# Kernel tuning notes

Measured on AMD Instinct MI355X. Metric: run time of the kernel, lower is better.

The kernel has to match this reference:

```python
import jax, jax.numpy as jnp
import numpy as np

HIDDEN = 1024


def setup_inputs() -> dict:
    key = jax.random.key(0)
    ks = jax.random.split(key, 8)
    x_in, y_in, out_dim, hidden = 1024, 1024, 1024, HIDDEN
    Nx, Ny = 4096, 4096
    s = lambda d: 1.0 / np.sqrt(d)
    return {
        "x": jax.random.normal(ks[0], (Nx, x_in), jnp.float32),
        "y": jax.random.normal(ks[1], (Ny, y_in), jnp.float32),
        "Wq": jax.random.normal(ks[2], (hidden, x_in), jnp.float32) * s(x_in),
        "bq": jnp.zeros((hidden,), jnp.float32),
        "Wk": jax.random.normal(ks[3], (hidden, y_in), jnp.float32) * s(y_in),
        "bk": jnp.zeros((hidden,), jnp.float32),
        "Wv": jax.random.normal(ks[4], (out_dim, y_in), jnp.float32) * s(y_in),
        "bv": jnp.zeros((out_dim,), jnp.float32),
    }


def reference(x, y, Wq, bq, Wk, bk, Wv, bv):
    # Linear projections (torch Linear: x @ W.T + b)
    q = x @ Wq.T + bq          # [Nx, H]
    k = y @ Wk.T + bk          # [Ny, H]
    v = y @ Wv.T + bv          # [Ny, D_out]
    scores = (q @ k.T) / jnp.sqrt(jnp.asarray(HIDDEN, q.dtype))  # [Nx, Ny]
    attn = jax.nn.softmax(scores, axis=1)
    return attn @ v            # [Nx, D_out]
```

## Files before the change

### kernel.cpp

```cpp
#include <hip/hip_runtime.h>
#include <cstdint>
#include <cstddef>

typedef __attribute__((ext_vector_type(8))) __bf16 bf16x8;
typedef __attribute__((ext_vector_type(4))) float  f32x4;

#define WAITCNT_VM(n) ((n & 0xF) | 0x70 | 0xF00 | (((n) >> 4) << 14))

__device__ __forceinline__ unsigned short f32_to_bf16(float f) {
    union { float f; unsigned int u; } cv;
    cv.f = f;
    unsigned int u = cv.u;
    return (unsigned short)((u + 0x7fffu + ((u >> 16) & 1u)) >> 16);
}

__device__ __forceinline__ float bf16_to_f32(unsigned short h) {
    union { unsigned int u; float f; } cv;
    cv.u = ((unsigned int)h) << 16;
    return cv.f;
}

__device__ __forceinline__ void async_copy16(const unsigned short* g, unsigned short* lds) {
    __builtin_amdgcn_global_load_lds(
        (const __attribute__((address_space(1))) unsigned int*)g,
        (__attribute__((address_space(3))) unsigned int*)lds,
        16, 0, 0);
}

__global__ __launch_bounds__(256) void cast_all(
    const float* __restrict__ x,  const float* __restrict__ y,
    const float* __restrict__ wq, const float* __restrict__ wk, const float* __restrict__ wv,
    unsigned short* __restrict__ xb,  unsigned short* __restrict__ yb,
    unsigned short* __restrict__ wqb, unsigned short* __restrict__ wkb,
    unsigned short* __restrict__ wvb, float* __restrict__ lsum)
{
    int b = blockIdx.x;
    if (b >= 11264) {
        float4 z = {0.f, 0.f, 0.f, 0.f};
#pragma unroll
        for (int t = 0; t < 4; ++t)
            ((float4*)lsum)[threadIdx.x * 4 + t] = z;
        return;
    }
    const float* s; unsigned short* d; int base;
    if      (b < 4096)  { s = x;  d = xb;  base = b; }
    else if (b < 8192)  { s = y;  d = yb;  base = b - 4096; }
    else if (b < 9216)  { s = wq; d = wqb; base = b - 8192; }
    else if (b < 10240) { s = wk; d = wkb; base = b - 9216; }
    else                { s = wv; d = wvb; base = b - 10240; }
    int i = base * 256 + threadIdx.x;
    float4 v = ((const float4*)s)[i];
    ushort4 o;
    o.x = f32_to_bf16(v.x);
    o.y = f32_to_bf16(v.y);
    o.z = f32_to_bf16(v.z);
    o.w = f32_to_bf16(v.w);
    ((ushort4*)d)[i] = o;
}

__device__ __forceinline__ void gemm_core_pf(
    const unsigned short* __restrict__ A, const unsigned short* __restrict__ B,
    int K, int rowBase, int colBase, int kBeg, int kEnd,
    unsigned short* ldsA, unsigned short* ldsB, f32x4 acc[4][4])
{
    const int tid  = threadIdx.x;
    const int lane = tid & 63;
    const int wave = tid >> 6;
    const int quad = lane >> 4;
    const int r    = lane & 15;
    const int wm   = wave >> 1;
    const int wn   = wave & 1;

    const int c1 = tid + 256;
    const long aOff0 = (long)(rowBase + (tid >> 2)) * K + (tid & 3) * 8;
    const long aOff1 = (long)(rowBase + (c1  >> 2)) * K + (c1  & 3) * 8;
    const long bOff0 = (long)(colBase + (tid >> 2)) * K + (tid & 3) * 8;
    const long bOff1 = (long)(colBase + (c1  >> 2)) * K + (c1  & 3) * 8;
    unsigned short* ldsA0 = ldsA + tid * 8;
    unsigned short* ldsA1 = ldsA + c1 * 8;
    unsigned short* ldsB0 = ldsB + tid * 8;
    unsigned short* ldsB1 = ldsB + c1 * 8;

    const int aReadOff = (wm * 64 + r) * 32 + quad * 8;
    const int bReadOff = (wn * 64 + r) * 32 + quad * 8;

    const int nSteps = (kEnd - kBeg) >> 5;

    async_copy16(A + aOff0 + kBeg, ldsA0);
    async_copy16(A + aOff1 + kBeg, ldsA1);
    async_copy16(B + bOff0 + kBeg, ldsB0);
    async_copy16(B + bOff1 + kBeg, ldsB1);

    for (int s = 0; s < nSteps; ++s) {
        const int cur = (s & 1) << 12;
        const int nxt = cur ^ 4096;
        __builtin_amdgcn_s_waitcnt(0);
        __syncthreads();
        if (s + 1 < nSteps) {
            const int kn = kBeg + ((s + 1) << 5);
            async_copy16(A + aOff0 + kn, ldsA0 + nxt);
            async_copy16(A + aOff1 + kn, ldsA1 + nxt);
            async_copy16(B + bOff0 + kn, ldsB0 + nxt);
            async_copy16(B + bOff1 + kn, ldsB1 + nxt);
        }
        bf16x8 af[4], bfr[4];
#pragma unroll
        for (int i = 0; i < 4; ++i)
            af[i] = *(const bf16x8*)(ldsA + cur + aReadOff + i * 16 * 32);
#pragma unroll
        for (int j = 0; j < 4; ++j)
            bfr[j] = *(const bf16x8*)(ldsB + cur + bReadOff + j * 16 * 32);
#pragma unroll
        for (int i = 0; i < 4; ++i)
#pragma unroll
            for (int j = 0; j < 4; ++j)
                acc[i][j] = __builtin_amdgcn_mfma_f32_16x16x32_bf16(af[i], bfr[j], acc[i][j], 0, 0, 0);
    }
}

__device__ __forceinline__ void gemm_core_pf2(
    const unsigned short* __restrict__ A, const unsigned short* __restrict__ B,
    int K, int rowBase, int colBase, int kBeg, int kEnd,
    unsigned short* ldsA, unsigned short* ldsB, f32x4 acc[4][4])
{
    const int tid  = threadIdx.x;
    const int lane = tid & 63;
    const int wave = tid >> 6;
    const int quad = lane >> 4;
    const int r    = lane & 15;
    const int wm   = wave >> 1;
    const int wn   = wave & 1;

    const int c1 = tid + 256;
    const long aOff0 = (long)(rowBase + (tid >> 2)) * K + (tid & 3) * 8;
    const long aOff1 = (long)(rowBase + (c1  >> 2)) * K + (c1  & 3) * 8;
    const long bOff0 = (long)(colBase + (tid >> 2)) * K + (tid & 3) * 8;
    const long bOff1 = (long)(colBase + (c1  >> 2)) * K + (c1  & 3) * 8;
    unsigned short* ldsA0 = ldsA + tid * 8;
    unsigned short* ldsA1 = ldsA + c1 * 8;
    unsigned short* ldsB0 = ldsB + tid * 8;
    unsigned short* ldsB1 = ldsB + c1 * 8;

    const int aReadOff = (wm * 64 + r) * 32 + quad * 8;
    const int bReadOff = (wn * 64 + r) * 32 + quad * 8;

    const int nSteps = (kEnd - kBeg) >> 5;

    async_copy16(A + aOff0 + kBeg, ldsA0);
    async_copy16(A + aOff1 + kBeg, ldsA1);
    async_copy16(B + bOff0 + kBeg, ldsB0);
    async_copy16(B + bOff1 + kBeg, ldsB1);
    if (nSteps > 1) {
        async_copy16(A + aOff0 + kBeg + 32, ldsA0 + 4096);
        async_copy16(A + aOff1 + kBeg + 32, ldsA1 + 4096);
        async_copy16(B + bOff0 + kBeg + 32, ldsB0 + 4096);
        async_copy16(B + bOff1 + kBeg + 32, ldsB1 + 4096);
    }

    int cur = 0;
    for (int s = 0; s < nSteps; ++s) {
        if (s + 1 < nSteps) __builtin_amdgcn_s_waitcnt(WAITCNT_VM(4));
        else                __builtin_amdgcn_s_waitcnt(WAITCNT_VM(0));
        __builtin_amdgcn_s_barrier();
        __builtin_amdgcn_sched_barrier(0);
        if (s + 2 < nSteps) {
            int nb = cur + 2; if (nb >= 3) nb -= 3;
            const int no = nb * 4096;
            const int kn = kBeg + ((s + 2) << 5);
            async_copy16(A + aOff0 + kn, ldsA0 + no);
            async_copy16(A + aOff1 + kn, ldsA1 + no);
            async_copy16(B + bOff0 + kn, ldsB0 + no);
            async_copy16(B + bOff1 + kn, ldsB1 + no);
        }
        const int co = cur * 4096;
        bf16x8 af[4], bfr[4];
#pragma unroll
        for (int i = 0; i < 4; ++i)
            af[i] = *(const bf16x8*)(ldsA + co + aReadOff + i * 16 * 32);
#pragma unroll
        for (int j = 0; j < 4; ++j)
            bfr[j] = *(const bf16x8*)(ldsB + co + bReadOff + j * 16 * 32);
#pragma unroll
        for (int i = 0; i < 4; ++i)
#pragma unroll
            for (int j = 0; j < 4; ++j)
                acc[i][j] = __builtin_amdgcn_mfma_f32_16x16x32_bf16(af[i], bfr[j], acc[i][j], 0, 0, 0);
        if (++cur == 3) cur = 0;
    }
}

__global__ __launch_bounds__(256, 2)
void proj_batched(const unsigned short* __restrict__ xb, const unsigned short* __restrict__ yb,
                  const unsigned short* __restrict__ wqb, const unsigned short* __restrict__ wkb,
                  const unsigned short* __restrict__ wvb,
                  unsigned short* __restrict__ q, unsigned short* __restrict__ k,
                  unsigned short* __restrict__ vt,
                  const float* __restrict__ bq, const float* __restrict__ bk,
                  const float* __restrict__ bv)
{
    __shared__ __align__(16) unsigned short ldsA[2 * 128 * 32];
    __shared__ __align__(16) unsigned short ldsB[2 * 128 * 32];

    const int b = blockIdx.x;
    const int z = b >> 8;
    const int rb = b & 255;

    const unsigned short *A, *B;
    unsigned short* C;
    const float* bias;
    int N, rowBase, colBase;
    bool biasPerRow;
    if (z == 0) {
        A = xb; B = wqb; C = q; bias = bq; N = 1024; biasPerRow = false;
        colBase = (rb >> 5) * 128; rowBase = (rb & 31) * 128;
    } else if (z == 1) {
        A = yb; B = wkb; C = k; bias = bk; N = 1024; biasPerRow = false;
        colBase = (rb >> 5) * 128; rowBase = (rb & 31) * 128;
    } else {
        A = wvb; B = yb; C = vt; bias = bv; N = 4096; biasPerRow = true;
        colBase = (rb >> 3) * 128; rowBase = (rb & 7) * 128;
    }

    f32x4 acc[4][4];
#pragma unroll
    for (int i = 0; i < 4; ++i)
#pragma unroll
        for (int j = 0; j < 4; ++j)
            acc[i][j] = (f32x4){0.f, 0.f, 0.f, 0.f};

    gemm_core_pf(A, B, 1024, rowBase, colBase, 0, 1024, ldsA, ldsB, acc);

    const int lane = threadIdx.x & 63;
    const int wave = threadIdx.x >> 6;
    const int quad = lane >> 4;
    const int r    = lane & 15;
    const int orow0 = rowBase + (wave >> 1) * 64 + quad * 4;
    const int ocol0 = colBase + (wave & 1) * 64 + r;

#pragma unroll
    for (int i = 0; i < 4; ++i)
#pragma unroll
        for (int e = 0; e < 4; ++e) {
            const int row = orow0 + i * 16 + e;
            const float brow = biasPerRow ? bias[row] : 0.f;
#pragma unroll
            for (int j = 0; j < 4; ++j) {
                const int col = ocol0 + j * 16;
                const float bb = biasPerRow ? brow : bias[col];
                C[(long)row * N + col] = f32_to_bf16(acc[i][j][e] + bb);
            }
        }
}

__global__ __launch_bounds__(256, 2)
void scores_gemm(const unsigned short* __restrict__ q, const unsigned short* __restrict__ k,
                 unsigned short* __restrict__ P, float* __restrict__ lsum, float scale2)
{
    __shared__ __align__(16) unsigned short ldsA[2 * 128 * 32];
    __shared__ __align__(16) unsigned short ldsB[2 * 128 * 32];

    const int rowBase = blockIdx.y * 128;
    const int colBase = blockIdx.x * 128;

    f32x4 acc[4][4];
#pragma unroll
    for (int i = 0; i < 4; ++i)
#pragma unroll
        for (int j = 0; j < 4; ++j)
            acc[i][j] = (f32x4){0.f, 0.f, 0.f, 0.f};

    gemm_core_pf(q, k, 1024, rowBase, colBase, 0, 1024, ldsA, ldsB, acc);

    const int lane = threadIdx.x & 63;
    const int wave = threadIdx.x >> 6;
    const int quad = lane >> 4;
    const int r    = lane & 15;
    const int orow0 = rowBase + (wave >> 1) * 64 + quad * 4;
    const int ocol0 = colBase + (wave & 1) * 64 + r;

#pragma unroll
    for (int i = 0; i < 4; ++i)
#pragma unroll
        for (int e = 0; e < 4; ++e) {
            const int row = orow0 + i * 16 + e;
            float rs = 0.f;
#pragma unroll
            for (int j = 0; j < 4; ++j) {
                const int col = ocol0 + j * 16;
                const float p = exp2f(acc[i][j][e] * scale2);
                rs += p;
                P[(long)row * 4096 + col] = f32_to_bf16(p);
            }
#pragma unroll
            for (int m = 1; m < 16; m <<= 1) rs += __shfl_xor(rs, m, 64);
            if (r == 0) atomicAdd(&lsum[row], rs);
        }
}

template <int ATOMIC>
__global__ __launch_bounds__(256, 2)
void out_gemm_splitk(const unsigned short* __restrict__ P, const unsigned short* __restrict__ vt,
                     void* __restrict__ Out)
{
    __shared__ __align__(16) unsigned short ldsA[3 * 128 * 32];
    __shared__ __align__(16) unsigned short ldsB[3 * 128 * 32];

    const int bid = blockIdx.x;
    const int xt  = bid >> 6;
    const int yz  = bid & 63;
    const int yt  = yz >> 1;
    const int zt  = yz & 1;

    const int rowBase = yt * 128;
    const int colBase = xt * 128;
    const int kBeg = zt * 2048;

    f32x4 acc[4][4];
#pragma unroll
    for (int i = 0; i < 4; ++i)
#pragma unroll
        for (int j = 0; j < 4; ++j)
            acc[i][j] = (f32x4){0.f, 0.f, 0.f, 0.f};

    gemm_core_pf2(P, vt, 4096, rowBase, colBase, kBeg, kBeg + 2048, ldsA, ldsB, acc);

    const int lane = threadIdx.x & 63;
    const int wave = threadIdx.x >> 6;
    const int quad = lane >> 4;
    const int r    = lane & 15;
    const int orow0 = rowBase + (wave >> 1) * 64 + quad * 4;
    const int ocol0 = colBase + (wave & 1) * 64 + r;

#pragma unroll
    for (int i = 0; i < 4; ++i)
#pragma unroll
        for (int e = 0; e < 4; ++e) {
            const int row = orow0 + i * 16 + e;
#pragma unroll
            for (int j = 0; j < 4; ++j) {
                const int col = ocol0 + j * 16;
                if (ATOMIC) {
                    atomicAdd(&((float*)Out)[(long)row * 1024 + col], acc[i][j][e]);
                } else {
                    unsigned short* parts = (unsigned short*)Out + (size_t)zt * (4096 * 1024);
                    parts[(long)row * 1024 + col] = f32_to_bf16(acc[i][j][e]);
                }
            }
        }
}

__global__ __launch_bounds__(256) void reduce_norm(const unsigned short* __restrict__ parts,
                                                   const float* __restrict__ lsum,
                                                   float* __restrict__ O) {
    const int i = blockIdx.x * 256 + threadIdx.x;
    const float inv = 1.0f / lsum[i >> 8];
    const size_t stride = (size_t)(4096 * 1024) / 4;
    ushort4 a = ((const ushort4*)parts)[i];
    ushort4 b = ((const ushort4*)parts)[i + stride];
    float4 o;
    o.x = (bf16_to_f32(a.x) + bf16_to_f32(b.x)) * inv;
    o.y = (bf16_to_f32(a.y) + bf16_to_f32(b.y)) * inv;
    o.z = (bf16_to_f32(a.z) + bf16_to_f32(b.z)) * inv;
    o.w = (bf16_to_f32(a.w) + bf16_to_f32(b.w)) * inv;
    ((float4*)O)[i] = o;
}

__global__ __launch_bounds__(256) void norm_rows(float* __restrict__ O, const float* __restrict__ lsum) {
    int i = blockIdx.x * 256 + threadIdx.x;
    const float inv = 1.0f / lsum[i >> 8];
    float4 v = ((const float4*)O)[i];
    v.x *= inv; v.y *= inv; v.z *= inv; v.w *= inv;
    ((float4*)O)[i] = v;
}

extern "C" void kernel_launch(void* const* d_in, const int* in_sizes, int n_in,
                              void* d_out, int out_size, void* d_ws, size_t ws_size,
                              hipStream_t stream) {
    const float* x  = (const float*)d_in[0];
    const float* y  = (const float*)d_in[1];
    const float* Wq = (const float*)d_in[2];
    const float* bq = (const float*)d_in[3];
    const float* Wk = (const float*)d_in[4];
    const float* bk = (const float*)d_in[5];
    const float* Wv = (const float*)d_in[6];
    const float* bv = (const float*)d_in[7];

    constexpr int Nx = 4096, Ny = 4096, H = 1024, Dv = 1024, Kin = 1024;

    char* ws = (char*)d_ws;
    size_t off = 0;
    auto carve = [&](size_t bytes) {
        char* p = ws + off;
        off += (bytes + 255) & ~(size_t)255;
        return p;
    };

    unsigned short* q_bf  = (unsigned short*)carve((size_t)Nx * H * 2);
    unsigned short* k_bf  = (unsigned short*)carve((size_t)Ny * H * 2);
    unsigned short* vt_bf = (unsigned short*)carve((size_t)Dv * Ny * 2);
    float*          lsum  = (float*)carve((size_t)Nx * sizeof(float));

    char* overlay = ws + off;
    unsigned short* x_bf  = (unsigned short*)overlay;
    unsigned short* y_bf  = x_bf  + (size_t)Nx * Kin;
    unsigned short* Wq_bf = y_bf  + (size_t)Ny * Kin;
    unsigned short* Wk_bf = Wq_bf + (size_t)H  * Kin;
    unsigned short* Wv_bf = Wk_bf + (size_t)H  * Kin;
    unsigned short* P_bf  = (unsigned short*)overlay;

    const size_t overlay_bytes = (size_t)Nx * Ny * 2;
    unsigned short* parts = (unsigned short*)(overlay + overlay_bytes);
    const size_t need_parts = (overlay + overlay_bytes + 2 * (size_t)Nx * Dv * 2) - ws;
    const bool useParts = ws_size >= need_parts;

    if (!useParts)
        hipMemsetAsync(d_out, 0, (size_t)Nx * Dv * sizeof(float), stream);

    cast_all<<<11265, 256, 0, stream>>>(x, y, Wq, Wk, Wv, x_bf, y_bf, Wq_bf, Wk_bf, Wv_bf, lsum);

    proj_batched<<<768, 256, 0, stream>>>(x_bf, y_bf, Wq_bf, Wk_bf, Wv_bf,
                                          q_bf, k_bf, vt_bf, bq, bk, bv);

    const float scale2 = 1.4426950408889634f / 32.0f;
    scores_gemm<<<dim3(Ny / 128, Nx / 128), 256, 0, stream>>>(q_bf, k_bf, P_bf, lsum, scale2);

    if (useParts) {
        out_gemm_splitk<0><<<512, 256, 0, stream>>>(P_bf, vt_bf, parts);
        reduce_norm<<<Nx * Dv / 4 / 256, 256, 0, stream>>>(parts, lsum, (float*)d_out);
    } else {
        out_gemm_splitk<1><<<512, 256, 0, stream>>>(P_bf, vt_bf, d_out);
        norm_rows<<<Nx * Dv / 4 / 256, 256, 0, stream>>>((float*)d_out, lsum);
    }
}
```

Before: 235.8 us.

## Use 256x256-tile 8-wave GEMM core for scores and output GEMMs

Replaces the 128x128 tile GEMMs for the score and output products with a 256x256 tile, 512-thread core. It uses XOR-swizzled LDS, staggered half-tile async staging interleaved with MFMA phases, s_setprio, and block-index swizzling for L2 locality. The output GEMM moves from 2-way to 4-way split-K, so the reduction kernel now sums four bf16 partial buffers. This aims to raise arithmetic intensity and cut global/LDS traffic per MFMA. In exchange it uses more registers and LDS, leaves fewer blocks to fill the CUs, and needs more workspace for partials.

```diff
diff --git a/kernel.cpp b/kernel.cpp
--- a/kernel.cpp
+++ b/kernel.cpp
@@ -6,6 +6,7 @@
 typedef __attribute__((ext_vector_type(4))) float  f32x4;
 
 #define WAITCNT_VM(n) ((n & 0xF) | 0x70 | 0xF00 | (((n) >> 4) << 14))
+#define WAITCNT_LGKM0 (0xF | 0x70 | (3 << 14))
 
 __device__ __forceinline__ unsigned short f32_to_bf16(float f) {
     union { float f; unsigned int u; } cv;
@@ -118,77 +119,6 @@
     }
 }
 
-__device__ __forceinline__ void gemm_core_pf2(
-    const unsigned short* __restrict__ A, const unsigned short* __restrict__ B,
-    int K, int rowBase, int colBase, int kBeg, int kEnd,
-    unsigned short* ldsA, unsigned short* ldsB, f32x4 acc[4][4])
-{
-    const int tid  = threadIdx.x;
-    const int lane = tid & 63;
-    const int wave = tid >> 6;
-    const int quad = lane >> 4;
-    const int r    = lane & 15;
-    const int wm   = wave >> 1;
-    const int wn   = wave & 1;
-
-    const int c1 = tid + 256;
-    const long aOff0 = (long)(rowBase + (tid >> 2)) * K + (tid & 3) * 8;
-    const long aOff1 = (long)(rowBase + (c1  >> 2)) * K + (c1  & 3) * 8;
-    const long bOff0 = (long)(colBase + (tid >> 2)) * K + (tid & 3) * 8;
-    const long bOff1 = (long)(colBase + (c1  >> 2)) * K + (c1  & 3) * 8;
-    unsigned short* ldsA0 = ldsA + tid * 8;
-    unsigned short* ldsA1 = ldsA + c1 * 8;
-    unsigned short* ldsB0 = ldsB + tid * 8;
-    unsigned short* ldsB1 = ldsB + c1 * 8;
-
-    const int aReadOff = (wm * 64 + r) * 32 + quad * 8;
-    const int bReadOff = (wn * 64 + r) * 32 + quad * 8;
-
-    const int nSteps = (kEnd - kBeg) >> 5;
-
-    async_copy16(A + aOff0 + kBeg, ldsA0);
-    async_copy16(A + aOff1 + kBeg, ldsA1);
-    async_copy16(B + bOff0 + kBeg, ldsB0);
-    async_copy16(B + bOff1 + kBeg, ldsB1);
-    if (nSteps > 1) {
-        async_copy16(A + aOff0 + kBeg + 32, ldsA0 + 4096);
-        async_copy16(A + aOff1 + kBeg + 32, ldsA1 + 4096);
-        async_copy16(B + bOff0 + kBeg + 32, ldsB0 + 4096);
-        async_copy16(B + bOff1 + kBeg + 32, ldsB1 + 4096);
-    }
-
-    int cur = 0;
-    for (int s = 0; s < nSteps; ++s) {
-        if (s + 1 < nSteps) __builtin_amdgcn_s_waitcnt(WAITCNT_VM(4));
-        else                __builtin_amdgcn_s_waitcnt(WAITCNT_VM(0));
-        __builtin_amdgcn_s_barrier();
-        __builtin_amdgcn_sched_barrier(0);
-        if (s + 2 < nSteps) {
-            int nb = cur + 2; if (nb >= 3) nb -= 3;
-            const int no = nb * 4096;
-            const int kn = kBeg + ((s + 2) << 5);
-            async_copy16(A + aOff0 + kn, ldsA0 + no);
-            async_copy16(A + aOff1 + kn, ldsA1 + no);
-            async_copy16(B + bOff0 + kn, ldsB0 + no);
-            async_copy16(B + bOff1 + kn, ldsB1 + no);
-        }
-        const int co = cur * 4096;
-        bf16x8 af[4], bfr[4];
-#pragma unroll
-        for (int i = 0; i < 4; ++i)
-            af[i] = *(const bf16x8*)(ldsA + co + aReadOff + i * 16 * 32);
-#pragma unroll
-        for (int j = 0; j < 4; ++j)
-            bfr[j] = *(const bf16x8*)(ldsB + co + bReadOff + j * 16 * 32);
-#pragma unroll
-        for (int i = 0; i < 4; ++i)
-#pragma unroll
-            for (int j = 0; j < 4; ++j)
-                acc[i][j] = __builtin_amdgcn_mfma_f32_16x16x32_bf16(af[i], bfr[j], acc[i][j], 0, 0, 0);
-        if (++cur == 3) cur = 0;
-    }
-}
-
 __global__ __launch_bounds__(256, 2)
 void proj_batched(const unsigned short* __restrict__ xb, const unsigned short* __restrict__ yb,
                   const unsigned short* __restrict__ wqb, const unsigned short* __restrict__ wkb,
@@ -252,44 +182,161 @@
         }
 }
 
-__global__ __launch_bounds__(256, 2)
-void scores_gemm(const unsigned short* __restrict__ q, const unsigned short* __restrict__ k,
-                 unsigned short* __restrict__ P, float* __restrict__ lsum, float scale2)
-{
-    __shared__ __align__(16) unsigned short ldsA[2 * 128 * 32];
-    __shared__ __align__(16) unsigned short ldsB[2 * 128 * 32];
-
-    const int rowBase = blockIdx.y * 128;
-    const int colBase = blockIdx.x * 128;
-
-    f32x4 acc[4][4];
-#pragma unroll
-    for (int i = 0; i < 4; ++i)
-#pragma unroll
-        for (int j = 0; j < 4; ++j)
-            acc[i][j] = (f32x4){0.f, 0.f, 0.f, 0.f};
-
-    gemm_core_pf(q, k, 1024, rowBase, colBase, 0, 1024, ldsA, ldsB, acc);
-
-    const int lane = threadIdx.x & 63;
-    const int wave = threadIdx.x >> 6;
+__device__ __forceinline__ void stage_half(const unsigned short* src, long rstep,
+                                           unsigned short* ldsLane) {
+    async_copy16(src, ldsLane);
+    async_copy16(src + rstep, ldsLane + 4096);
+}
+
+__device__ __forceinline__ void gemm256_core(
+    const unsigned short* __restrict__ A, const unsigned short* __restrict__ B,
+    int K, int rowBase, int colBase, int kBeg, int nTiles,
+    unsigned short* lds, f32x4 acc[8][4])
+{
+    const int tid  = threadIdx.x;
+    const int lane = tid & 63;
+    const int wid  = tid >> 6;
     const int quad = lane >> 4;
     const int r    = lane & 15;
-    const int orow0 = rowBase + (wave >> 1) * 64 + quad * 4;
-    const int ocol0 = colBase + (wave & 1) * 64 + r;
-
-#pragma unroll
-    for (int i = 0; i < 4; ++i)
+    const int wm   = wid >> 2;
+    const int wn   = wid & 3;
+
+    const int row0 = tid >> 3;
+    const int chs8 = (((tid & 7) ^ (row0 & 7)) << 3);
+    const unsigned short* As = A + (long)(rowBase + row0) * K + chs8 + kBeg;
+    const unsigned short* Bs = B + (long)(colBase + row0) * K + chs8 + kBeg;
+    const long rstep = (long)K * 64;
+    const long hstep = (long)K * 128;
+    unsigned short* ldsLane = lds + tid * 8;
+
+    const int aRd = (wm << 13) + (r << 6);
+    const int bRd = 16384 + (wn << 12) + (r << 6);
+    const int sw0 = ((quad ^ (r & 7)) << 3);
+    const int sw1 = (((quad + 4) ^ (r & 7)) << 3);
+
+    stage_half(As,         rstep, ldsLane);
+    stage_half(As + hstep, rstep, ldsLane + 8192);
+    stage_half(Bs,         rstep, ldsLane + 16384);
+    stage_half(Bs + hstep, rstep, ldsLane + 24576);
+    if (nTiles > 1) {
+        stage_half(As + 64,         rstep, ldsLane + 32768);
+        stage_half(As + hstep + 64, rstep, ldsLane + 40960);
+    }
+    __builtin_amdgcn_s_waitcnt(WAITCNT_VM(4));
+    __builtin_amdgcn_s_barrier();
+    __builtin_amdgcn_sched_barrier(0);
+
+    for (int T = 0; T < nTiles; ++T) {
+        const int cur = (T & 1) << 15;
+        const int nxt = cur ^ 32768;
+
+        bf16x8 a0[8], b0[4];
+        if (T + 1 < nTiles) stage_half(Bs + (T + 1) * 64, rstep, ldsLane + nxt + 16384);
+#pragma unroll
+        for (int i = 0; i < 8; ++i)
+            a0[i] = *(const bf16x8*)(lds + cur + aRd + i * 1024 + sw0);
+#pragma unroll
+        for (int j = 0; j < 4; ++j)
+            b0[j] = *(const bf16x8*)(lds + cur + bRd + j * 1024 + sw0);
+        __builtin_amdgcn_s_barrier();
+        __builtin_amdgcn_s_waitcnt(WAITCNT_LGKM0);
+        __builtin_amdgcn_sched_barrier(0);
+        __builtin_amdgcn_s_setprio(1);
+#pragma unroll
+        for (int i = 0; i < 4; ++i)
+#pragma unroll
+            for (int j = 0; j < 4; ++j)
+                acc[i][j] = __builtin_amdgcn_mfma_f32_16x16x32_bf16(a0[i], b0[j], acc[i][j], 0, 0, 0);
+        __builtin_amdgcn_s_setprio(0);
+        __builtin_amdgcn_s_barrier();
+
+        if (T + 1 < nTiles) stage_half(Bs + hstep + (T + 1) * 64, rstep, ldsLane + nxt + 24576);
+        __builtin_amdgcn_s_setprio(1);
+#pragma unroll
+        for (int i = 4; i < 8; ++i)
+#pragma unroll
+            for (int j = 0; j < 4; ++j)
+                acc[i][j] = __builtin_amdgcn_mfma_f32_16x16x32_bf16(a0[i], b0[j], acc[i][j], 0, 0, 0);
+        __builtin_amdgcn_s_setprio(0);
+        __builtin_amdgcn_s_barrier();
+
+        bf16x8 a1[8], b1[4];
+#pragma unroll
+        for (int i = 0; i < 8; ++i)
+            a1[i] = *(const bf16x8*)(lds + cur + aRd + i * 1024 + sw1);
+#pragma unroll
+        for (int j = 0; j < 4; ++j)
+            b1[j] = *(const bf16x8*)(lds + cur + bRd + j * 1024 + sw1);
+        __builtin_amdgcn_s_barrier();
+        __builtin_amdgcn_s_waitcnt(WAITCNT_LGKM0);
+        __builtin_amdgcn_sched_barrier(0);
+        __builtin_amdgcn_s_setprio(1);
+#pragma unroll
+        for (int i = 0; i < 4; ++i)
+#pragma unroll
+            for (int j = 0; j < 4; ++j)
+                acc[i][j] = __builtin_amdgcn_mfma_f32_16x16x32_bf16(a1[i], b1[j], acc[i][j], 0, 0, 0);
+        __builtin_amdgcn_s_setprio(0);
+        __builtin_amdgcn_s_barrier();
+
+        if (T + 2 < nTiles) {
+            stage_half(As + (T + 2) * 64,         rstep, ldsLane + cur);
+            stage_half(As + hstep + (T + 2) * 64, rstep, ldsLane + cur + 8192);
+        }
+        __builtin_amdgcn_s_setprio(1);
+#pragma unroll
+        for (int i = 4; i < 8; ++i)
+#pragma unroll
+            for (int j = 0; j < 4; ++j)
+                acc[i][j] = __builtin_amdgcn_mfma_f32_16x16x32_bf16(a1[i], b1[j], acc[i][j], 0, 0, 0);
+        __builtin_amdgcn_s_setprio(0);
+
+        if (T + 2 < nTiles) __builtin_amdgcn_s_waitcnt(WAITCNT_VM(4));
+        else                __builtin_amdgcn_s_waitcnt(WAITCNT_VM(0));
+        __builtin_amdgcn_s_barrier();
+        __builtin_amdgcn_sched_barrier(0);
+    }
+}
+
+__global__ __launch_bounds__(512, 2)
+void scores_gemm256(const unsigned short* __restrict__ q, const unsigned short* __restrict__ k,
+                    unsigned short* __restrict__ P, float* __restrict__ lsum, float scale2)
+{
+    __shared__ __align__(16) unsigned short lds[2 * 32768];
+
+    const int bid = blockIdx.x;
+    const int swz = (bid & 7) * 32 + (bid >> 3);
+    const int mt = swz >> 4, nt = swz & 15;
+    const int rowBase = mt * 256;
+    const int colBase = nt * 256;
+
+    f32x4 acc[8][4];
+#pragma unroll
+    for (int i = 0; i < 8; ++i)
+#pragma unroll
+        for (int j = 0; j < 4; ++j)
+            acc[i][j] = (f32x4){0.f, 0.f, 0.f, 0.f};
+
+    gemm256_core(q, k, 1024, rowBase, colBase, 0, 16, lds, acc);
+
+    const int lane = threadIdx.x & 63;
+    const int wid  = threadIdx.x >> 6;
+    const int quad = lane >> 4;
+    const int r    = lane & 15;
+    const int orow0 = rowBase + (wid >> 2) * 128 + quad * 4;
+    const int ocol0 = colBase + (wid & 3) * 64 + r;
+
+#pragma unroll
+    for (int mi = 0; mi < 8; ++mi)
 #pragma unroll
         for (int e = 0; e < 4; ++e) {
-            const int row = orow0 + i * 16 + e;
+            const int row = orow0 + mi * 16 + e;
             float rs = 0.f;
 #pragma unroll
-            for (int j = 0; j < 4; ++j) {
-                const int col = ocol0 + j * 16;
-                const float p = exp2f(acc[i][j][e] * scale2);
+            for (int nj = 0; nj < 4; ++nj) {
+                const float p = exp2f(acc[mi][nj][e] * scale2);
                 rs += p;
-                P[(long)row * 4096 + col] = f32_to_bf16(p);
+                P[(long)row * 4096 + ocol0 + nj * 16] = f32_to_bf16(p);
             }
 #pragma unroll
             for (int m = 1; m < 16; m <<= 1) rs += __shfl_xor(rs, m, 64);
@@ -298,70 +345,70 @@
 }
 
 template <int ATOMIC>
-__global__ __launch_bounds__(256, 2)
-void out_gemm_splitk(const unsigned short* __restrict__ P, const unsigned short* __restrict__ vt,
-                     void* __restrict__ Out)
-{
-    __shared__ __align__(16) unsigned short ldsA[3 * 128 * 32];
-    __shared__ __align__(16) unsigned short ldsB[3 * 128 * 32];
+__global__ __launch_bounds__(512, 2)
+void out_gemm256(const unsigned short* __restrict__ P, const unsigned short* __restrict__ vt,
+                 void* __restrict__ Out)
+{
+    __shared__ __align__(16) unsigned short lds[2 * 32768];
 
     const int bid = blockIdx.x;
-    const int xt  = bid >> 6;
-    const int yz  = bid & 63;
-    const int yt  = yz >> 1;
-    const int zt  = yz & 1;
-
-    const int rowBase = yt * 128;
-    const int colBase = xt * 128;
-    const int kBeg = zt * 2048;
-
-    f32x4 acc[4][4];
-#pragma unroll
-    for (int i = 0; i < 4; ++i)
+    const int swz = (bid & 7) * 32 + (bid >> 3);
+    const int z  = swz & 3;
+    const int nt = (swz >> 2) & 3;
+    const int mt = swz >> 4;
+    const int rowBase = mt * 256;
+    const int colBase = nt * 256;
+    const int kBeg = z * 1024;
+
+    f32x4 acc[8][4];
+#pragma unroll
+    for (int i = 0; i < 8; ++i)
 #pragma unroll
         for (int j = 0; j < 4; ++j)
             acc[i][j] = (f32x4){0.f, 0.f, 0.f, 0.f};
 
-    gemm_core_pf2(P, vt, 4096, rowBase, colBase, kBeg, kBeg + 2048, ldsA, ldsB, acc);
+    gemm256_core(P, vt, 4096, rowBase, colBase, kBeg, 16, lds, acc);
 
     const int lane = threadIdx.x & 63;
-    const int wave = threadIdx.x >> 6;
+    const int wid  = threadIdx.x >> 6;
     const int quad = lane >> 4;
     const int r    = lane & 15;
-    const int orow0 = rowBase + (wave >> 1) * 64 + quad * 4;
-    const int ocol0 = colBase + (wave & 1) * 64 + r;
-
-#pragma unroll
-    for (int i = 0; i < 4; ++i)
+    const int orow0 = rowBase + (wid >> 2) * 128 + quad * 4;
+    const int ocol0 = colBase + (wid & 3) * 64 + r;
+
+#pragma unroll
+    for (int mi = 0; mi < 8; ++mi)
 #pragma unroll
         for (int e = 0; e < 4; ++e) {
-            const int row = orow0 + i * 16 + e;
-#pragma unroll
-            for (int j = 0; j < 4; ++j) {
-                const int col = ocol0 + j * 16;
+            const int row = orow0 + mi * 16 + e;
+#pragma unroll
+            for (int nj = 0; nj < 4; ++nj) {
+                const int col = ocol0 + nj * 16;
                 if (ATOMIC) {
-                    atomicAdd(&((float*)Out)[(long)row * 1024 + col], acc[i][j][e]);
+                    atomicAdd(&((float*)Out)[(long)row * 1024 + col], acc[mi][nj][e]);
                 } else {
-                    unsigned short* parts = (unsigned short*)Out + (size_t)zt * (4096 * 1024);
-                    parts[(long)row * 1024 + col] = f32_to_bf16(acc[i][j][e]);
+                    unsigned short* parts = (unsigned short*)Out + (size_t)z * (4096 * 1024);
+                    parts[(long)row * 1024 + col] = f32_to_bf16(acc[mi][nj][e]);
                 }
             }
         }
 }
 
-__global__ __launch_bounds__(256) void reduce_norm(const unsigned short* __restrict__ parts,
-                                                   const float* __restrict__ lsum,
-                                                   float* __restrict__ O) {
+__global__ __launch_bounds__(256) void reduce_norm4(const unsigned short* __restrict__ parts,
+                                                    const float* __restrict__ lsum,
+                                                    float* __restrict__ O) {
     const int i = blockIdx.x * 256 + threadIdx.x;
     const float inv = 1.0f / lsum[i >> 8];
     const size_t stride = (size_t)(4096 * 1024) / 4;
     ushort4 a = ((const ushort4*)parts)[i];
     ushort4 b = ((const ushort4*)parts)[i + stride];
+    ushort4 c = ((const ushort4*)parts)[i + 2 * stride];
+    ushort4 d = ((const ushort4*)parts)[i + 3 * stride];
     float4 o;
-    o.x = (bf16_to_f32(a.x) + bf16_to_f32(b.x)) * inv;
-    o.y = (bf16_to_f32(a.y) + bf16_to_f32(b.y)) * inv;
-    o.z = (bf16_to_f32(a.z) + bf16_to_f32(b.z)) * inv;
-    o.w = (bf16_to_f32(a.w) + bf16_to_f32(b.w)) * inv;
+    o.x = (bf16_to_f32(a.x) + bf16_to_f32(b.x) + bf16_to_f32(c.x) + bf16_to_f32(d.x)) * inv;
+    o.y = (bf16_to_f32(a.y) + bf16_to_f32(b.y) + bf16_to_f32(c.y) + bf16_to_f32(d.y)) * inv;
+    o.z = (bf16_to_f32(a.z) + bf16_to_f32(b.z) + bf16_to_f32(c.z) + bf16_to_f32(d.z)) * inv;
+    o.w = (bf16_to_f32(a.w) + bf16_to_f32(b.w) + bf16_to_f32(c.w) + bf16_to_f32(d.w)) * inv;
     ((float4*)O)[i] = o;
 }
 
@@ -409,8 +456,9 @@
     unsigned short* P_bf  = (unsigned short*)overlay;
 
     const size_t overlay_bytes = (size_t)Nx * Ny * 2;
+    const size_t partsBytes = (size_t)Nx * Dv * 2;
     unsigned short* parts = (unsigned short*)(overlay + overlay_bytes);
-    const size_t need_parts = (overlay + overlay_bytes + 2 * (size_t)Nx * Dv * 2) - ws;
+    const size_t need_parts = (size_t)((overlay + overlay_bytes + 4 * partsBytes) - ws);
     const bool useParts = ws_size >= need_parts;
 
     if (!useParts)
@@ -422,13 +470,13 @@
                                           q_bf, k_bf, vt_bf, bq, bk, bv);
 
     const float scale2 = 1.4426950408889634f / 32.0f;
-    scores_gemm<<<dim3(Ny / 128, Nx / 128), 256, 0, stream>>>(q_bf, k_bf, P_bf, lsum, scale2);
+    scores_gemm256<<<256, 512, 0, stream>>>(q_bf, k_bf, P_bf, lsum, scale2);
 
     if (useParts) {
-        out_gemm_splitk<0><<<512, 256, 0, stream>>>(P_bf, vt_bf, parts);
-        reduce_norm<<<Nx * Dv / 4 / 256, 256, 0, stream>>>(parts, lsum, (float*)d_out);
+        out_gemm256<0><<<256, 512, 0, stream>>>(P_bf, vt_bf, parts);
+        reduce_norm4<<<(Nx * Dv / 4) / 256, 256, 0, stream>>>(parts, lsum, (float*)d_out);
     } else {
-        out_gemm_splitk<1><<<512, 256, 0, stream>>>(P_bf, vt_bf, d_out);
+        out_gemm256<1><<<256, 512, 0, stream>>>(P_bf, vt_bf, d_out);
         norm_rows<<<Nx * Dv / 4 / 256, 256, 0, stream>>>((float*)d_out, lsum);
     }
 }
```

Result: faster. 223.4 us (-5.3%).
